# Optimization experiments

Measured on AMD Instinct MI355X. Metric: run time of the kernel, lower is better.

The kernel has to match this reference:

```python
import jax, jax.numpy as jnp
import numpy as np

HID = 101
IN = 3


def lstm_cell(x, h, c, W_ih, W_hh, b_ih, b_hh):
    # PyTorch LSTMCell gate order: i, f, g, o
    gates = x @ W_ih.T + b_ih + h @ W_hh.T + b_hh  # [B, 4H]
    i, f, g, o = jnp.split(gates, 4, axis=-1)
    i = jax.nn.sigmoid(i)
    f = jax.nn.sigmoid(f)
    g = jnp.tanh(g)
    o = jax.nn.sigmoid(o)
    c_new = f * c + i * g
    h_new = o * jnp.tanh(c_new)
    return h_new, c_new


def setup_inputs() -> dict:
    key = jax.random.key(0)
    ks = jax.random.split(key, 12)
    B, T = 1024, 256
    s1 = 1.0 / np.sqrt(HID)
    u = lambda k, shp: jax.random.uniform(k, shp, jnp.float32, -s1, s1)
    return {
        "input": jax.random.normal(ks[0], (B, T, IN), jnp.float32),
        "W_ih1": u(ks[1], (4 * HID, IN)),
        "W_hh1": u(ks[2], (4 * HID, HID)),
        "b_ih1": u(ks[3], (4 * HID,)),
        "b_hh1": u(ks[4], (4 * HID,)),
        "W_ih2": u(ks[5], (4 * HID, HID)),
        "W_hh2": u(ks[6], (4 * HID, HID)),
        "b_ih2": u(ks[7], (4 * HID,)),
        "b_hh2": u(ks[8], (4 * HID,)),
        "Wl": u(ks[9], (IN, HID)),
        "bl": u(ks[10], (IN,)),
        "future": 32,
    }


def reference(input, W_ih1, W_hh1, b_ih1, b_hh1, W_ih2, W_hh2, b_ih2, b_hh2, Wl, bl, future):
    B = input.shape[0]
    h1 = jnp.zeros((B, HID), input.dtype)
    c1 = jnp.zeros((B, HID), input.dtype)
    h2 = jnp.zeros((B, HID), input.dtype)
    c2 = jnp.zeros((B, HID), input.dtype)

    def step(carry, x_t):
        h1, c1, h2, c2 = carry
        h1, c1 = lstm_cell(x_t, h1, c1, W_ih1, W_hh1, b_ih1, b_hh1)
        h2, c2 = lstm_cell(h1, h2, c2, W_ih2, W_hh2, b_ih2, b_hh2)
        out = h2 @ Wl.T + bl  # [B, 3]
        return (h1, c1, h2, c2), out

    xs = jnp.transpose(input, (1, 0, 2))  # [T, B, 3]
    carry, outs = jax.lax.scan(step, (h1, c1, h2, c2), xs)

    if future > 0:
        last_out = outs[-1]

        def fstep(carry, _):
            h1, c1, h2, c2, out = carry
            h1, c1 = lstm_cell(out, h1, c1, W_ih1, W_hh1, b_ih1, b_hh1)
            h2, c2 = lstm_cell(h1, h2, c2, W_ih2, W_hh2, b_ih2, b_hh2)
            out = h2 @ Wl.T + bl
            return (h1, c1, h2, c2, out), out

        _, fouts = jax.lax.scan(fstep, (*carry, last_out), None, length=future)
        outs = jnp.concatenate([outs, fouts], axis=0)

    return jnp.transpose(outs, (1, 0, 2))  # [B, T+future, 3]
```

## Files before the change

kernel.cpp:

```cpp
#include <hip/hip_runtime.h>
#include <hip/hip_bf16.h>

#define HID 101
#define BATCH 1024
#define RPB 4
#define NBLK 256
#define NTHR 512

#define A1SZ  (7*4*4*512)
#define A2SZ  (7*4*7*512)
#define A2OFF A1SZ
#define AOOFF (A1SZ + A2SZ)
#define AOSZ  (4*512)

typedef _Float16 h8 __attribute__((ext_vector_type(8)));
typedef float f4 __attribute__((ext_vector_type(4)));

__global__ void prep_kernel(const float* __restrict__ W_ih1, const float* __restrict__ W_hh1,
                            const float* __restrict__ b_ih1, const float* __restrict__ b_hh1,
                            const float* __restrict__ W_ih2, const float* __restrict__ W_hh2,
                            const float* __restrict__ b_ih2, const float* __restrict__ b_hh2,
                            const float* __restrict__ Wl, _Float16* __restrict__ wsA) {
    int idx = blockIdx.x * blockDim.x + threadIdx.x;
    int stride = gridDim.x * blockDim.x;
    for (int t = idx; t < A1SZ; t += stride) {
        int i = t & 7, lane = (t >> 3) & 63, kt = (t >> 9) & 3, tau = (t >> 11) & 3, w = t >> 13;
        int k = kt * 32 + ((lane >> 4) & 3) * 8 + i;
        int u = 16 * w + (lane & 15);
        float v = 0.f;
        if (u < HID) {
            int g = tau * HID + u;
            if (k < HID) v = W_hh1[g * HID + k];
            else if (k >= 101 && k <= 103) v = W_ih1[g * 3 + (k - 101)];
            else if (k == 104) v = b_ih1[g] + b_hh1[g];
        }
        wsA[t] = (_Float16)v;
    }
    for (int t = idx; t < A2SZ; t += stride) {
        int i = t & 7, lane = (t >> 3) & 63;
        int rem = t >> 9;
        int kt = rem % 7; rem /= 7;
        int tau = rem & 3, w = rem >> 2;
        int k = kt * 32 + ((lane >> 4) & 3) * 8 + i;
        int u = 16 * w + (lane & 15);
        float v = 0.f;
        if (u < HID) {
            int g = tau * HID + u;
            if (k < HID) v = W_ih2[g * HID + k];
            else if (k == 104) v = b_ih2[g] + b_hh2[g];
            else if (k >= 112 && k < 213) v = W_hh2[g * HID + (k - 112)];
        }
        wsA[A2OFF + t] = (_Float16)v;
    }
    for (int t = idx; t < AOSZ; t += stride) {
        int i = t & 7, lane = (t >> 3) & 63, kk = (t >> 9) & 3;
        int k = (kk + 3) * 32 + ((lane >> 4) & 3) * 8 + i;
        int j = lane & 15;
        float v = (j < 3 && k >= 112 && k < 213) ? Wl[j * HID + (k - 112)] : 0.f;
        wsA[AOOFF + t] = (_Float16)v;
    }
}

__device__ __forceinline__ float sigm(float z) {
    return __builtin_amdgcn_rcpf(1.f + __expf(-z));
}
__device__ __forceinline__ float tanhf_(float z) {
    return 1.f - 2.f * __builtin_amdgcn_rcpf(__expf(2.f * z) + 1.f);
}

__global__ __launch_bounds__(NTHR, 2) void lstm_kernel(
    const float* __restrict__ input, const _Float16* __restrict__ wsA,
    const float* __restrict__ bl, int T, int steps, float* __restrict__ out)
{
    const int tid = threadIdx.x;
    const int wid = tid >> 6, lane = tid & 63;
    const int q = lane >> 4, col = lane & 15;
    const int r0 = blockIdx.x * RPB;
    const int ostride = steps * 3;

    __shared__ _Float16 Sb[2][3584];
    __shared__ float zw[7][4][4][16];

    h8 A1[4][4];
    h8 A2[4][7];
    if (wid < 7) {
        #pragma unroll
        for (int tau = 0; tau < 4; tau++) {
            #pragma unroll
            for (int kt = 0; kt < 4; kt++)
                A1[tau][kt] = *(const volatile h8*)(
                    wsA + ((size_t)((wid * 4 + tau) * 4 + kt) * 512 + lane * 8));
            #pragma unroll
            for (int kt = 0; kt < 7; kt++)
                A2[tau][kt] = *(const volatile h8*)(
                    wsA + (size_t)A2OFF + ((size_t)((wid * 4 + tau) * 7 + kt) * 512 + lane * 8));
        }
    } else {
        #pragma unroll
        for (int kt = 0; kt < 4; kt++)
            A2[0][kt] = *(const volatile h8*)(
                wsA + (size_t)AOOFF + ((size_t)(kt) * 512 + lane * 8));
    }
    const float bl0 = bl[0], bl1 = bl[1], bl2 = bl[2];

    const int r_ew = lane & 3, ul = lane >> 2;
    const int u = 16 * wid + ul;
    const bool ewv = (wid < 7) && (u < HID);
    const int hs1 = (u >> 3) * 128 + r_ew * 8 + (u & 7);
    const int hs2 = (14 + (u >> 3)) * 128 + r_ew * 8 + (u & 7);
    const int boff = (q * 16 + col) * 8;
    const int xr = lane / 3, xj = lane - 3 * xr;
    const int xoff = 12 * 128 + xr * 8 + 5 + xj;

    for (int i2 = tid; i2 < 3584; i2 += NTHR) {
        Sb[0][i2] = (_Float16)0.f; Sb[1][i2] = (_Float16)0.f;
    }
    __syncthreads();
    if (tid < 16) {
        Sb[0][13 * 128 + tid * 8] = (_Float16)1.0f;
        Sb[1][13 * 128 + tid * 8] = (_Float16)1.0f;
    }
    if (tid < 12) {
        int r = tid / 3, j = tid - 3 * (tid / 3);
        Sb[1][12 * 128 + r * 8 + 5 + j] = (_Float16)input[(size_t)(r0 + r) * T * 3 + j];
    }
    float c1 = 0.f, c2 = 0.f;
    __syncthreads();

    auto STEP = [&](int t, _Float16* R, _Float16* W, bool fut) {
        float xv = 0.f;
        if (fut) {
            if (wid == 7) {
                f4 ao = {0.f, 0.f, 0.f, 0.f};
                #pragma unroll
                for (int kk = 0; kk < 4; kk++) {
                    h8 b = *(const h8*)(W + (kk + 3) * 512 + boff);
                    ao = __builtin_amdgcn_mfma_f32_16x16x32_f16(A2[0][kk], b, ao, 0, 0, 0);
                }
                if (lane < 4) {
                    float o0 = ao[0] + bl0, o1 = ao[1] + bl1, o2 = ao[2] + bl2;
                    float* op = out + (size_t)(r0 + lane) * ostride + (size_t)(t - 1) * 3;
                    op[0] = o0; op[1] = o1; op[2] = o2;
                    R[12 * 128 + lane * 8 + 5] = (_Float16)o0;
                    R[12 * 128 + lane * 8 + 6] = (_Float16)o1;
                    R[12 * 128 + lane * 8 + 7] = (_Float16)o2;
                }
            }
            __syncthreads();
        }
        if (wid < 7) {
            f4 acc0 = {0.f,0.f,0.f,0.f}, acc1 = acc0, acc2 = acc0, acc3 = acc0;
            #pragma unroll
            for (int kt = 0; kt < 4; kt++) {
                h8 b = *(const h8*)(R + kt * 512 + boff);
                acc0 = __builtin_amdgcn_mfma_f32_16x16x32_f16(A1[0][kt], b, acc0, 0, 0, 0);
                acc1 = __builtin_amdgcn_mfma_f32_16x16x32_f16(A1[1][kt], b, acc1, 0, 0, 0);
                acc2 = __builtin_amdgcn_mfma_f32_16x16x32_f16(A1[2][kt], b, acc2, 0, 0, 0);
                acc3 = __builtin_amdgcn_mfma_f32_16x16x32_f16(A1[3][kt], b, acc3, 0, 0, 0);
            }
            if (col < 4) {
                *(f4*)&zw[wid][0][col][4 * q] = acc0;
                *(f4*)&zw[wid][1][col][4 * q] = acc1;
                *(f4*)&zw[wid][2][col][4 * q] = acc2;
                *(f4*)&zw[wid][3][col][4 * q] = acc3;
            }
            float z0 = zw[wid][0][r_ew][ul], z1 = zw[wid][1][r_ew][ul];
            float z2 = zw[wid][2][r_ew][ul], z3 = zw[wid][3][r_ew][ul];
            float ig = sigm(z0), fg = sigm(z1), gg = tanhf_(z2), og = sigm(z3);
            c1 = fg * c1 + ig * gg;
            float h1v = og * tanhf_(c1);
            if (ewv) W[hs1] = (_Float16)h1v;
        } else {
            if (!fut) {
                if (t > 0) {
                    f4 ao = {0.f, 0.f, 0.f, 0.f};
                    #pragma unroll
                    for (int kk = 0; kk < 4; kk++) {
                        h8 b = *(const h8*)(W + (kk + 3) * 512 + boff);
                        ao = __builtin_amdgcn_mfma_f32_16x16x32_f16(A2[0][kk], b, ao, 0, 0, 0);
                    }
                    if (lane < 4) {
                        float* op = out + (size_t)(r0 + lane) * ostride + (size_t)(t - 1) * 3;
                        op[0] = ao[0] + bl0; op[1] = ao[1] + bl1; op[2] = ao[2] + bl2;
                    }
                }
                if (t + 1 < T && lane < 12)
                    xv = input[(size_t)(r0 + xr) * T * 3 + (size_t)(t + 1) * 3 + xj];
            }
        }
        __syncthreads();
        if (wid < 7) {
            f4 acc0 = {0.f,0.f,0.f,0.f}, acc1 = acc0, acc2 = acc0, acc3 = acc0;
            #pragma unroll
            for (int kt = 0; kt < 7; kt++) {
                h8 b = *(const h8*)(W + kt * 512 + boff);
                acc0 = __builtin_amdgcn_mfma_f32_16x16x32_f16(A2[0][kt], b, acc0, 0, 0, 0);
                acc1 = __builtin_amdgcn_mfma_f32_16x16x32_f16(A2[1][kt], b, acc1, 0, 0, 0);
                acc2 = __builtin_amdgcn_mfma_f32_16x16x32_f16(A2[2][kt], b, acc2, 0, 0, 0);
                acc3 = __builtin_amdgcn_mfma_f32_16x16x32_f16(A2[3][kt], b, acc3, 0, 0, 0);
            }
            if (col < 4) {
                *(f4*)&zw[wid][0][col][4 * q] = acc0;
                *(f4*)&zw[wid][1][col][4 * q] = acc1;
                *(f4*)&zw[wid][2][col][4 * q] = acc2;
                *(f4*)&zw[wid][3][col][4 * q] = acc3;
            }
            float z0 = zw[wid][0][r_ew][ul], z1 = zw[wid][1][r_ew][ul];
            float z2 = zw[wid][2][r_ew][ul], z3 = zw[wid][3][r_ew][ul];
            float ig = sigm(z0), fg = sigm(z1), gg = tanhf_(z2), og = sigm(z3);
            c2 = fg * c2 + ig * gg;
            float h2v = og * tanhf_(c2);
            if (ewv) R[hs2] = (_Float16)h2v;
        } else {
            if (!fut && t + 1 < T && lane < 12)
                W[xoff] = (_Float16)xv;
        }
        __syncthreads();
    };

    for (int t = 0; t < T; t += 2) {
        STEP(t,     Sb[1], Sb[0], false);
        STEP(t + 1, Sb[0], Sb[1], false);
    }
    for (int t = T; t < steps; t += 2) {
        STEP(t,     Sb[1], Sb[0], true);
        STEP(t + 1, Sb[0], Sb[1], true);
    }
    if (wid == 7) {
        f4 ao = {0.f, 0.f, 0.f, 0.f};
        #pragma unroll
        for (int kk = 0; kk < 4; kk++) {
            h8 b = *(const h8*)(&Sb[0][0] + (kk + 3) * 512 + boff);
            ao = __builtin_amdgcn_mfma_f32_16x16x32_f16(A2[0][kk], b, ao, 0, 0, 0);
        }
        if (lane < 4) {
            float* op = out + (size_t)(r0 + lane) * ostride + (size_t)(steps - 1) * 3;
            op[0] = ao[0] + bl0; op[1] = ao[1] + bl1; op[2] = ao[2] + bl2;
        }
    }
}

extern "C" void kernel_launch(void* const* d_in, const int* in_sizes, int n_in,
                              void* d_out, int out_size, void* d_ws, size_t ws_size,
                              hipStream_t stream) {
    const float* input = (const float*)d_in[0];
    const float* W_ih1 = (const float*)d_in[1];
    const float* W_hh1 = (const float*)d_in[2];
    const float* b_ih1 = (const float*)d_in[3];
    const float* b_hh1 = (const float*)d_in[4];
    const float* W_ih2 = (const float*)d_in[5];
    const float* W_hh2 = (const float*)d_in[6];
    const float* b_ih2 = (const float*)d_in[7];
    const float* b_hh2 = (const float*)d_in[8];
    const float* Wl    = (const float*)d_in[9];
    const float* bl    = (const float*)d_in[10];
    int T = in_sizes[0] / (BATCH * 3);
    int steps = out_size / (BATCH * 3);
    _Float16* wsA = (_Float16*)d_ws;

    hipLaunchKernelGGL(prep_kernel, dim3(512), dim3(256), 0, stream,
                       W_ih1, W_hh1, b_ih1, b_hh1, W_ih2, W_hh2, b_ih2, b_hh2, Wl, wsA);
    hipLaunchKernelGGL(lstm_kernel, dim3(NBLK), dim3(NTHR), 0, stream,
                       input, wsA, bl, T, steps, (float*)d_out);
}
```

Baseline: 472.9 us.

## Wavefront-pipeline the two LSTM layers to halve barriers per teacher-forced step

```diff
diff --git a/kernel.cpp b/kernel.cpp
--- a/kernel.cpp
+++ b/kernel.cpp
@@ -6,6 +6,7 @@
 #define RPB 4
 #define NBLK 256
 #define NTHR 512
+#define TSEQ 256
 
 #define A1SZ  (7*4*4*512)
 #define A2SZ  (7*4*7*512)
@@ -68,9 +69,11 @@
     return 1.f - 2.f * __builtin_amdgcn_rcpf(__expf(2.f * z) + 1.f);
 }
 
+#define MFMA(acc, a, b) acc = __builtin_amdgcn_mfma_f32_16x16x32_f16(a, b, acc, 0, 0, 0)
+
 __global__ __launch_bounds__(NTHR, 2) void lstm_kernel(
     const float* __restrict__ input, const _Float16* __restrict__ wsA,
-    const float* __restrict__ bl, int T, int steps, float* __restrict__ out)
+    const float* __restrict__ bl, int steps, float* __restrict__ out)
 {
     const int tid = threadIdx.x;
     const int wid = tid >> 6, lane = tid & 63;
@@ -79,7 +82,9 @@
     const int ostride = steps * 3;
 
     __shared__ _Float16 Sb[2][3584];
-    __shared__ float zw[7][4][4][16];
+    __shared__ float zwA[7][4][4][16];
+    __shared__ float zwB[7][4][4][16];
+    __shared__ _Float16 xpre[TSEQ * 12];
 
     h8 A1[4][4];
     h8 A2[4][7];
@@ -108,12 +113,17 @@
     const bool ewv = (wid < 7) && (u < HID);
     const int hs1 = (u >> 3) * 128 + r_ew * 8 + (u & 7);
     const int hs2 = (14 + (u >> 3)) * 128 + r_ew * 8 + (u & 7);
-    const int boff = (q * 16 + col) * 8;
+    const int boff = q * 128 + col * 8;
     const int xr = lane / 3, xj = lane - 3 * xr;
     const int xoff = 12 * 128 + xr * 8 + 5 + xj;
 
     for (int i2 = tid; i2 < 3584; i2 += NTHR) {
         Sb[0][i2] = (_Float16)0.f; Sb[1][i2] = (_Float16)0.f;
+    }
+    for (int g = tid; g < RPB * TSEQ * 3; g += NTHR) {
+        int r = g / (TSEQ * 3), rem = g - r * (TSEQ * 3);
+        int tt = rem / 3, j = rem - 3 * tt;
+        xpre[tt * 12 + r * 3 + j] = (_Float16)input[(size_t)(r0 + r) * (TSEQ * 3) + rem];
     }
     __syncthreads();
     if (tid < 16) {
@@ -122,116 +132,216 @@
     }
     if (tid < 12) {
         int r = tid / 3, j = tid - 3 * (tid / 3);
-        Sb[1][12 * 128 + r * 8 + 5 + j] = (_Float16)input[(size_t)(r0 + r) * T * 3 + j];
+        Sb[0][12 * 128 + r * 8 + 5 + j] = xpre[r * 3 + j];
     }
     float c1 = 0.f, c2 = 0.f;
     __syncthreads();
 
-    auto STEP = [&](int t, _Float16* R, _Float16* W, bool fut) {
-        float xv = 0.f;
-        if (fut) {
-            if (wid == 7) {
+    for (int t = 0; t < TSEQ; ++t) {
+        _Float16* Rb = Sb[t & 1];
+        _Float16* Wt = Sb[1 - (t & 1)];
+        if (wid < 7) {
+            h8 bf0 = (_Float16)0.f, bf1 = bf0, bf2 = bf0, bf3 = bf0,
+               bf4 = bf0, bf5 = bf0, bf6 = bf0;
+            if (col < 4) {
+                bf0 = *(const h8*)(Rb + 0 * 512 + boff);
+                bf1 = *(const h8*)(Rb + 1 * 512 + boff);
+                bf2 = *(const h8*)(Rb + 2 * 512 + boff);
+                bf3 = *(const h8*)(Rb + 3 * 512 + boff);
+                bf4 = *(const h8*)(Rb + 4 * 512 + boff);
+                bf5 = *(const h8*)(Rb + 5 * 512 + boff);
+                bf6 = *(const h8*)(Rb + 6 * 512 + boff);
+            }
+            f4 a0 = {0.f,0.f,0.f,0.f}, a1 = a0, a2 = a0, a3 = a0;
+            MFMA(a0, A1[0][0], bf0); MFMA(a1, A1[1][0], bf0); MFMA(a2, A1[2][0], bf0); MFMA(a3, A1[3][0], bf0);
+            MFMA(a0, A1[0][1], bf1); MFMA(a1, A1[1][1], bf1); MFMA(a2, A1[2][1], bf1); MFMA(a3, A1[3][1], bf1);
+            MFMA(a0, A1[0][2], bf2); MFMA(a1, A1[1][2], bf2); MFMA(a2, A1[2][2], bf2); MFMA(a3, A1[3][2], bf2);
+            MFMA(a0, A1[0][3], bf3); MFMA(a1, A1[1][3], bf3); MFMA(a2, A1[2][3], bf3); MFMA(a3, A1[3][3], bf3);
+            if (col < 4) {
+                *(f4*)&zwA[wid][0][col][4 * q] = a0;
+                *(f4*)&zwA[wid][1][col][4 * q] = a1;
+                *(f4*)&zwA[wid][2][col][4 * q] = a2;
+                *(f4*)&zwA[wid][3][col][4 * q] = a3;
+            }
+            if (t >= 1) {
+                f4 b0 = {0.f,0.f,0.f,0.f}, b1 = b0, b2 = b0, b3 = b0;
+                MFMA(b0, A2[0][0], bf0); MFMA(b1, A2[1][0], bf0); MFMA(b2, A2[2][0], bf0); MFMA(b3, A2[3][0], bf0);
+                MFMA(b0, A2[0][1], bf1); MFMA(b1, A2[1][1], bf1); MFMA(b2, A2[2][1], bf1); MFMA(b3, A2[3][1], bf1);
+                MFMA(b0, A2[0][2], bf2); MFMA(b1, A2[1][2], bf2); MFMA(b2, A2[2][2], bf2); MFMA(b3, A2[3][2], bf2);
+                MFMA(b0, A2[0][3], bf3); MFMA(b1, A2[1][3], bf3); MFMA(b2, A2[2][3], bf3); MFMA(b3, A2[3][3], bf3);
+                MFMA(b0, A2[0][4], bf4); MFMA(b1, A2[1][4], bf4); MFMA(b2, A2[2][4], bf4); MFMA(b3, A2[3][4], bf4);
+                MFMA(b0, A2[0][5], bf5); MFMA(b1, A2[1][5], bf5); MFMA(b2, A2[2][5], bf5); MFMA(b3, A2[3][5], bf5);
+                MFMA(b0, A2[0][6], bf6); MFMA(b1, A2[1][6], bf6); MFMA(b2, A2[2][6], bf6); MFMA(b3, A2[3][6], bf6);
+                if (col < 4) {
+                    *(f4*)&zwB[wid][0][col][4 * q] = b0;
+                    *(f4*)&zwB[wid][1][col][4 * q] = b1;
+                    *(f4*)&zwB[wid][2][col][4 * q] = b2;
+                    *(f4*)&zwB[wid][3][col][4 * q] = b3;
+                }
+            }
+            {
+                float z0 = zwA[wid][0][r_ew][ul], z1 = zwA[wid][1][r_ew][ul];
+                float z2 = zwA[wid][2][r_ew][ul], z3 = zwA[wid][3][r_ew][ul];
+                float ig = sigm(z0), fg = sigm(z1), gg = tanhf_(z2), og = sigm(z3);
+                c1 = fg * c1 + ig * gg;
+                float h1v = og * tanhf_(c1);
+                if (ewv) Wt[hs1] = (_Float16)h1v;
+            }
+            if (t >= 1) {
+                float z0 = zwB[wid][0][r_ew][ul], z1 = zwB[wid][1][r_ew][ul];
+                float z2 = zwB[wid][2][r_ew][ul], z3 = zwB[wid][3][r_ew][ul];
+                float ig = sigm(z0), fg = sigm(z1), gg = tanhf_(z2), og = sigm(z3);
+                c2 = fg * c2 + ig * gg;
+                float h2v = og * tanhf_(c2);
+                if (ewv) Wt[hs2] = (_Float16)h2v;
+            }
+        } else {
+            if (t >= 2) {
                 f4 ao = {0.f, 0.f, 0.f, 0.f};
                 #pragma unroll
                 for (int kk = 0; kk < 4; kk++) {
-                    h8 b = *(const h8*)(W + (kk + 3) * 512 + boff);
-                    ao = __builtin_amdgcn_mfma_f32_16x16x32_f16(A2[0][kk], b, ao, 0, 0, 0);
+                    h8 b = (_Float16)0.f;
+                    if (col < 4) b = *(const h8*)(Rb + (kk + 3) * 512 + boff);
+                    MFMA(ao, A2[0][kk], b);
                 }
                 if (lane < 4) {
-                    float o0 = ao[0] + bl0, o1 = ao[1] + bl1, o2 = ao[2] + bl2;
-                    float* op = out + (size_t)(r0 + lane) * ostride + (size_t)(t - 1) * 3;
-                    op[0] = o0; op[1] = o1; op[2] = o2;
-                    R[12 * 128 + lane * 8 + 5] = (_Float16)o0;
-                    R[12 * 128 + lane * 8 + 6] = (_Float16)o1;
-                    R[12 * 128 + lane * 8 + 7] = (_Float16)o2;
+                    float* op = out + (size_t)(r0 + lane) * ostride + (size_t)(t - 2) * 3;
+                    op[0] = ao[0] + bl0; op[1] = ao[1] + bl1; op[2] = ao[2] + bl2;
                 }
             }
-            __syncthreads();
-        }
+            if (t + 1 < TSEQ && lane < 12)
+                Wt[xoff] = xpre[(t + 1) * 12 + xr * 3 + xj];
+        }
+        __syncthreads();
+    }
+
+    {
+        _Float16* Rb = Sb[0];
+        _Float16* Wt = Sb[1];
         if (wid < 7) {
-            f4 acc0 = {0.f,0.f,0.f,0.f}, acc1 = acc0, acc2 = acc0, acc3 = acc0;
+            h8 bf0 = (_Float16)0.f, bf1 = bf0, bf2 = bf0, bf3 = bf0,
+               bf4 = bf0, bf5 = bf0, bf6 = bf0;
+            if (col < 4) {
+                bf0 = *(const h8*)(Rb + 0 * 512 + boff);
+                bf1 = *(const h8*)(Rb + 1 * 512 + boff);
+                bf2 = *(const h8*)(Rb + 2 * 512 + boff);
+                bf3 = *(const h8*)(Rb + 3 * 512 + boff);
+                bf4 = *(const h8*)(Rb + 4 * 512 + boff);
+                bf5 = *(const h8*)(Rb + 5 * 512 + boff);
+                bf6 = *(const h8*)(Rb + 6 * 512 + boff);
+            }
+            f4 b0 = {0.f,0.f,0.f,0.f}, b1 = b0, b2 = b0, b3 = b0;
+            MFMA(b0, A2[0][0], bf0); MFMA(b1, A2[1][0], bf0); MFMA(b2, A2[2][0], bf0); MFMA(b3, A2[3][0], bf0);
+            MFMA(b0, A2[0][1], bf1); MFMA(b1, A2[1][1], bf1); MFMA(b2, A2[2][1], bf1); MFMA(b3, A2[3][1], bf1);
+            MFMA(b0, A2[0][2], bf2); MFMA(b1, A2[1][2], bf2); MFMA(b2, A2[2][2], bf2); MFMA(b3, A2[3][2], bf2);
+            MFMA(b0, A2[0][3], bf3); MFMA(b1, A2[1][3], bf3); MFMA(b2, A2[2][3], bf3); MFMA(b3, A2[3][3], bf3);
+            MFMA(b0, A2[0][4], bf4); MFMA(b1, A2[1][4], bf4); MFMA(b2, A2[2][4], bf4); MFMA(b3, A2[3][4], bf4);
+            MFMA(b0, A2[0][5], bf5); MFMA(b1, A2[1][5], bf5); MFMA(b2, A2[2][5], bf5); MFMA(b3, A2[3][5], bf5);
+            MFMA(b0, A2[0][6], bf6); MFMA(b1, A2[1][6], bf6); MFMA(b2, A2[2][6], bf6); MFMA(b3, A2[3][6], bf6);
+            if (col < 4) {
+                *(f4*)&zwB[wid][0][col][4 * q] = b0;
+                *(f4*)&zwB[wid][1][col][4 * q] = b1;
+                *(f4*)&zwB[wid][2][col][4 * q] = b2;
+                *(f4*)&zwB[wid][3][col][4 * q] = b3;
+            }
+            float z0 = zwB[wid][0][r_ew][ul], z1 = zwB[wid][1][r_ew][ul];
+            float z2 = zwB[wid][2][r_ew][ul], z3 = zwB[wid][3][r_ew][ul];
+            float ig = sigm(z0), fg = sigm(z1), gg = tanhf_(z2), og = sigm(z3);
+            c2 = fg * c2 + ig * gg;
+            float h2v = og * tanhf_(c2);
+            if (ewv) Wt[hs2] = (_Float16)h2v;
+        } else {
+            f4 ao = {0.f, 0.f, 0.f, 0.f};
+            #pragma unroll
+            for (int kk = 0; kk < 4; kk++) {
+                h8 b = (_Float16)0.f;
+                if (col < 4) b = *(const h8*)(Rb + (kk + 3) * 512 + boff);
+                MFMA(ao, A2[0][kk], b);
+            }
+            if (lane < 4) {
+                float* op = out + (size_t)(r0 + lane) * ostride + (size_t)(TSEQ - 2) * 3;
+                op[0] = ao[0] + bl0; op[1] = ao[1] + bl1; op[2] = ao[2] + bl2;
+            }
+        }
+        __syncthreads();
+    }
+
+    for (int t = TSEQ; t < steps; ++t) {
+        _Float16* R = Sb[t & 1];
+        _Float16* W = Sb[1 - (t & 1)];
+        if (wid == 7) {
+            f4 ao = {0.f, 0.f, 0.f, 0.f};
+            #pragma unroll
+            for (int kk = 0; kk < 4; kk++) {
+                h8 b = (_Float16)0.f;
+                if (col < 4) b = *(const h8*)(W + (kk + 3) * 512 + boff);
+                MFMA(ao, A2[0][kk], b);
+            }
+            if (lane < 4) {
+                float o0 = ao[0] + bl0, o1 = ao[1] + bl1, o2 = ao[2] + bl2;
+                float* op = out + (size_t)(r0 + lane) * ostride + (size_t)(t - 1) * 3;
+                op[0] = o0; op[1] = o1; op[2] = o2;
+                R[12 * 128 + lane * 8 + 5] = (_Float16)o0;
+                R[12 * 128 + lane * 8 + 6] = (_Float16)o1;
+                R[12 * 128 + lane * 8 + 7] = (_Float16)o2;
+            }
+        }
+        __syncthreads();
+        if (wid < 7) {
+            f4 a0 = {0.f,0.f,0.f,0.f}, a1 = a0, a2 = a0, a3 = a0;
             #pragma unroll
             for (int kt = 0; kt < 4; kt++) {
-                h8 b = *(const h8*)(R + kt * 512 + boff);
-                acc0 = __builtin_amdgcn_mfma_f32_16x16x32_f16(A1[0][kt], b, acc0, 0, 0, 0);
-                acc1 = __builtin_amdgcn_mfma_f32_16x16x32_f16(A1[1][kt], b, acc1, 0, 0, 0);
-                acc2 = __builtin_amdgcn_mfma_f32_16x16x32_f16(A1[2][kt], b, acc2, 0, 0, 0);
-                acc3 = __builtin_amdgcn_mfma_f32_16x16x32_f16(A1[3][kt], b, acc3, 0, 0, 0);
-            }
-            if (col < 4) {
-                *(f4*)&zw[wid][0][col][4 * q] = acc0;
-                *(f4*)&zw[wid][1][col][4 * q] = acc1;
-                *(f4*)&zw[wid][2][col][4 * q] = acc2;
-                *(f4*)&zw[wid][3][col][4 * q] = acc3;
-            }
-            float z0 = zw[wid][0][r_ew][ul], z1 = zw[wid][1][r_ew][ul];
-            float z2 = zw[wid][2][r_ew][ul], z3 = zw[wid][3][r_ew][ul];
+                h8 b = (_Float16)0.f;
+                if (col < 4) b = *(const h8*)(R + kt * 512 + boff);
+                MFMA(a0, A1[0][kt], b); MFMA(a1, A1[1][kt], b);
+                MFMA(a2, A1[2][kt], b); MFMA(a3, A1[3][kt], b);
+            }
+            if (col < 4) {
+                *(f4*)&zwA[wid][0][col][4 * q] = a0;
+                *(f4*)&zwA[wid][1][col][4 * q] = a1;
+                *(f4*)&zwA[wid][2][col][4 * q] = a2;
+                *(f4*)&zwA[wid][3][col][4 * q] = a3;
+            }
+            float z0 = zwA[wid][0][r_ew][ul], z1 = zwA[wid][1][r_ew][ul];
+            float z2 = zwA[wid][2][r_ew][ul], z3 = zwA[wid][3][r_ew][ul];
             float ig = sigm(z0), fg = sigm(z1), gg = tanhf_(z2), og = sigm(z3);
             c1 = fg * c1 + ig * gg;
             float h1v = og * tanhf_(c1);
             if (ewv) W[hs1] = (_Float16)h1v;
-        } else {
-            if (!fut) {
-                if (t > 0) {
-                    f4 ao = {0.f, 0.f, 0.f, 0.f};
-                    #pragma unroll
-                    for (int kk = 0; kk < 4; kk++) {
-                        h8 b = *(const h8*)(W + (kk + 3) * 512 + boff);
-                        ao = __builtin_amdgcn_mfma_f32_16x16x32_f16(A2[0][kk], b, ao, 0, 0, 0);
-                    }
-                    if (lane < 4) {
-                        float* op = out + (size_t)(r0 + lane) * ostride + (size_t)(t - 1) * 3;
-                        op[0] = ao[0] + bl0; op[1] = ao[1] + bl1; op[2] = ao[2] + bl2;
-                    }
-                }
-                if (t + 1 < T && lane < 12)
-                    xv = input[(size_t)(r0 + xr) * T * 3 + (size_t)(t + 1) * 3 + xj];
-            }
         }
         __syncthreads();
         if (wid < 7) {
-            f4 acc0 = {0.f,0.f,0.f,0.f}, acc1 = acc0, acc2 = acc0, acc3 = acc0;
+            f4 b0 = {0.f,0.f,0.f,0.f}, b1 = b0, b2 = b0, b3 = b0;
             #pragma unroll
             for (int kt = 0; kt < 7; kt++) {
-                h8 b = *(const h8*)(W + kt * 512 + boff);
-                acc0 = __builtin_amdgcn_mfma_f32_16x16x32_f16(A2[0][kt], b, acc0, 0, 0, 0);
-                acc1 = __builtin_amdgcn_mfma_f32_16x16x32_f16(A2[1][kt], b, acc1, 0, 0, 0);
-                acc2 = __builtin_amdgcn_mfma_f32_16x16x32_f16(A2[2][kt], b, acc2, 0, 0, 0);
-                acc3 = __builtin_amdgcn_mfma_f32_16x16x32_f16(A2[3][kt], b, acc3, 0, 0, 0);
-            }
-            if (col < 4) {
-                *(f4*)&zw[wid][0][col][4 * q] = acc0;
-                *(f4*)&zw[wid][1][col][4 * q] = acc1;
-                *(f4*)&zw[wid][2][col][4 * q] = acc2;
-                *(f4*)&zw[wid][3][col][4 * q] = acc3;
-            }
-            float z0 = zw[wid][0][r_ew][ul], z1 = zw[wid][1][r_ew][ul];
-            float z2 = zw[wid][2][r_ew][ul], z3 = zw[wid][3][r_ew][ul];
+                h8 b = (_Float16)0.f;
+                if (col < 4) b = *(const h8*)(W + kt * 512 + boff);
+                MFMA(b0, A2[0][kt], b); MFMA(b1, A2[1][kt], b);
+                MFMA(b2, A2[2][kt], b); MFMA(b3, A2[3][kt], b);
+            }
+            if (col < 4) {
+                *(f4*)&zwB[wid][0][col][4 * q] = b0;
+                *(f4*)&zwB[wid][1][col][4 * q] = b1;
+                *(f4*)&zwB[wid][2][col][4 * q] = b2;
+                *(f4*)&zwB[wid][3][col][4 * q] = b3;
+            }
+            float z0 = zwB[wid][0][r_ew][ul], z1 = zwB[wid][1][r_ew][ul];
+            float z2 = zwB[wid][2][r_ew][ul], z3 = zwB[wid][3][r_ew][ul];
             float ig = sigm(z0), fg = sigm(z1), gg = tanhf_(z2), og = sigm(z3);
             c2 = fg * c2 + ig * gg;
             float h2v = og * tanhf_(c2);
             if (ewv) R[hs2] = (_Float16)h2v;
-        } else {
-            if (!fut && t + 1 < T && lane < 12)
-                W[xoff] = (_Float16)xv;
-        }
-        __syncthreads();
-    };
-
-    for (int t = 0; t < T; t += 2) {
-        STEP(t,     Sb[1], Sb[0], false);
-        STEP(t + 1, Sb[0], Sb[1], false);
-    }
-    for (int t = T; t < steps; t += 2) {
-        STEP(t,     Sb[1], Sb[0], true);
-        STEP(t + 1, Sb[0], Sb[1], true);
-    }
+        }
+        __syncthreads();
+    }
+
     if (wid == 7) {
         f4 ao = {0.f, 0.f, 0.f, 0.f};
         #pragma unroll
         for (int kk = 0; kk < 4; kk++) {
-            h8 b = *(const h8*)(&Sb[0][0] + (kk + 3) * 512 + boff);
-            ao = __builtin_amdgcn_mfma_f32_16x16x32_f16(A2[0][kk], b, ao, 0, 0, 0);
+            h8 b = (_Float16)0.f;
+            if (col < 4) b = *(const h8*)(&Sb[1][0] + (kk + 3) * 512 + boff);
+            MFMA(ao, A2[0][kk], b);
         }
         if (lane < 4) {
             float* op = out + (size_t)(r0 + lane) * ostride + (size_t)(steps - 1) * 3;
@@ -254,12 +364,11 @@
     const float* b_hh2 = (const float*)d_in[8];
     const float* Wl    = (const float*)d_in[9];
     const float* bl    = (const float*)d_in[10];
-    int T = in_sizes[0] / (BATCH * 3);
     int steps = out_size / (BATCH * 3);
     _Float16* wsA = (_Float16*)d_ws;
 
     hipLaunchKernelGGL(prep_kernel, dim3(512), dim3(256), 0, stream,
                        W_ih1, W_hh1, b_ih1, b_hh1, W_ih2, W_hh2, b_ih2, b_hh2, Wl, wsA);
     hipLaunchKernelGGL(lstm_kernel, dim3(NBLK), dim3(NTHR), 0, stream,
-                       input, wsA, bl, T, steps, (float*)d_out);
-}
+                       input, wsA, bl, steps, (float*)d_out);
+}
```

Result: faster. 398.0 us (-15.8%).
